# Kernel optimization log

Hardware: AMD Instinct MI355X
Metric: run time of the kernel (lower is better)

Reference implementation:

```python
import jax, jax.numpy as jnp
import numpy as np

B, D, H, E = 1024, 64, 128, 8192


def setup_inputs() -> dict:
    key = jax.random.key(0)
    ks = jax.random.split(key, 10)
    def w(k, shape, fan_in):
        return jax.random.normal(k, shape, jnp.float32) / np.float32(np.sqrt(fan_in))
    return {
        "mu": jax.random.normal(ks[0], (B, D), jnp.float32),
        "current_edge_index": jax.random.randint(ks[1], (2, E), 0, B),
        "W1": w(ks[2], (D, H), D),   "b1": jnp.zeros((H,), jnp.float32),
        "W2": w(ks[3], (H, H), H),   "b2": jnp.zeros((H,), jnp.float32),
        "Ws1": w(ks[4], (2 * H, H), 2 * H), "bs1": jnp.zeros((H,), jnp.float32),
        "Ws2": w(ks[5], (H, 1), H),  "bs2": jnp.zeros((1,), jnp.float32),
        "Wg1": w(ks[6], (2 * H, H), 2 * H), "bg1": jnp.zeros((H,), jnp.float32),
        "Wg2": w(ks[7], (H, D), H), "bg2": jnp.zeros((D,), jnp.float32),
    }


def _gcn(x, W, b, src, dst, n):
    loop = jnp.arange(n)
    s = jnp.concatenate([src, loop])
    d = jnp.concatenate([dst, loop])
    deg = jax.ops.segment_sum(jnp.ones_like(s, x.dtype), d, num_segments=n)
    dinv = jax.lax.rsqrt(jnp.maximum(deg, 1e-12))
    norm = dinv[s] * dinv[d]                      # [E+n]
    xw = x @ W                                    # [n,H]
    out = jax.ops.segment_sum(xw[s] * norm[:, None], d, num_segments=n)
    return out + b


def _pairwise_scores(h, Ws1, bs1, Ws2, bs2):
    # score_mlp([h_i || h_j]) for all pairs, vectorized: split first-layer weight
    A = h @ Ws1[:H]                               # [B,H] contribution of h_i
    C = h @ Ws1[H:]                               # [B,H] contribution of h_j
    pre = jax.nn.relu(A[:, None, :] + C[None, :, :] + bs1)   # [B,B,H]
    s = (pre @ Ws2)[..., 0] + bs2[0]              # [B,B]
    up = jnp.triu(s, 1)                           # only i<j computed in original
    return up + up.T                              # symmetric, zero diagonal


def _kruskal(scores_np, n):
    iu, ju = np.triu_indices(n, 1)
    w = scores_np[iu, ju]
    order = np.argsort(-w, kind="stable")         # descending, stable like list.sort
    parent = list(range(n))
    rank = [0] * n
    def find(u):
        while parent[u] != u:
            parent[u] = parent[parent[u]]
            u = parent[u]
        return u
    edges = []
    for k in order:
        i, j = int(iu[k]), int(ju[k])
        ri, rj = find(i), find(j)
        if ri == rj:
            continue
        if rank[ri] < rank[rj]:
            parent[ri] = rj
        elif rank[ri] > rank[rj]:
            parent[rj] = ri
        else:
            parent[rj] = ri
            rank[ri] += 1
        edges.append((i, j))
        if len(edges) == n - 1:
            break
    return np.asarray(edges, dtype=np.int64)      # [n-1, 2]


def reference(mu, current_edge_index, W1, b1, W2, b2, Ws1, bs1, Ws2, bs2, Wg1, bg1, Wg2, bg2):
    src, dst = current_edge_index[0], current_edge_index[1]
    h = jax.nn.relu(_gcn(mu, W1, b1, src, dst, B))
    h = jax.nn.relu(_gcn(h, W2, b2, src, dst, B))
    scores = _pairwise_scores(h, Ws1, bs1, Ws2, bs2)          # [B,B]
    mst = _kruskal(np.asarray(scores), B)                     # [B-1,2], i<j
    ei = jnp.asarray(mst[:, 0])
    ej = jnp.asarray(mst[:, 1])
    # bidirectional edge index: src=[i,j,...], dst=[j,i,...]
    new_edge_index = jnp.stack([
        jnp.stack([ei, ej], axis=1).reshape(-1),
        jnp.stack([ej, ei], axis=1).reshape(-1),
    ], axis=0)                                                # [2, 2*(B-1)]
    hp = jnp.concatenate([h[ei], h[ej]], axis=1)              # [B-1, 2H]
    gamma = jnp.tanh(jax.nn.relu(hp @ Wg1 + bg1) @ Wg2 + bg2) # [B-1, D]
    return (new_edge_index, gamma)
```

## Files before the change

### kernel.cpp

```cpp
#include <hip/hip_runtime.h>
#include <hip/hip_bf16.h>
#include <math.h>

#define BN 1024
#define DIN 64
#define HD 128
#define EN 8192
#define SLOTS_STRIDE 64
#define MMR 8
#define NC 128

typedef unsigned long long u64;

__global__ void k_init(int* cnt, int* comp, u64* best, int* mstcnt) {
    int i = blockIdx.x * blockDim.x + threadIdx.x;
    if (i < BN) { cnt[i] = 0; comp[i] = i; best[i] = 0ull; }
    if (i == 0) *mstcnt = 0;
}

__global__ void k_fill(const int* dst, int* cnt, int* slots) {
    int e = blockIdx.x * blockDim.x + threadIdx.x;
    if (e < EN) {
        int d = dst[e];
        int p = atomicAdd(&cnt[d], 1);
        if (p < SLOTS_STRIDE) slots[d * SLOTS_STRIDE + p] = e;
    }
}

__global__ __launch_bounds__(128) void k_finish(int* slots, const int* cnt, float* dinv) {
    __shared__ int buf[128][65];
    int tid = threadIdx.x;
    int t = blockIdx.x * 128 + tid;
    int n = cnt[t];
    if (n > SLOTS_STRIDE) n = SLOTS_STRIDE;
    for (int k = 0; k < n; k++) buf[tid][k] = slots[t * SLOTS_STRIDE + k];
    for (int k = 1; k < n; k++) {
        int v = buf[tid][k];
        int q = k - 1;
        while (q >= 0 && buf[tid][q] > v) { buf[tid][q + 1] = buf[tid][q]; q--; }
        buf[tid][q + 1] = v;
    }
    for (int k = 0; k < n; k++) slots[t * SLOTS_STRIDE + k] = buf[tid][k];
    dinv[t] = 1.0f / sqrtf(fmaxf((float)(n + 1), 1e-12f));
}

__global__ __launch_bounds__(128) void k_mm8(const float* x, const float* W, const float* bias,
                                             float* out, int K) {
    __shared__ float xr[MMR][HD];
    int col = threadIdx.x;
    int r0 = blockIdx.x * MMR;
#pragma unroll
    for (int r = 0; r < MMR; r++)
        if (col < K) xr[r][col] = x[(r0 + r) * K + col];
    __syncthreads();
    float b = bias ? bias[col] : 0.0f;
    float acc[MMR];
#pragma unroll
    for (int r = 0; r < MMR; r++) acc[r] = b;
#pragma unroll 4
    for (int k = 0; k < K; k++) {
        float w = W[k * HD + col];
#pragma unroll
        for (int r = 0; r < MMR; r++) acc[r] = fmaf(xr[r][k], w, acc[r]);
    }
#pragma unroll
    for (int r = 0; r < MMR; r++) out[(r0 + r) * HD + col] = acc[r];
}

__global__ __launch_bounds__(128) void k_mmAC(const float* h, const float* Ws1, const float* bs1,
                                              float* Aa, float* Cc) {
    __shared__ float xr[MMR][HD];
    int col = threadIdx.x;
    int r0 = blockIdx.x * MMR;
#pragma unroll
    for (int r = 0; r < MMR; r++) xr[r][col] = h[(r0 + r) * HD + col];
    __syncthreads();
    float accA[MMR], accC[MMR];
    float bc = bs1[col];
#pragma unroll
    for (int r = 0; r < MMR; r++) { accA[r] = 0.0f; accC[r] = bc; }
#pragma unroll 2
    for (int k = 0; k < HD; k++) {
        float wa = Ws1[k * HD + col];
        float wc = Ws1[(HD + k) * HD + col];
#pragma unroll
        for (int r = 0; r < MMR; r++) {
            accA[r] = fmaf(xr[r][k], wa, accA[r]);
            accC[r] = fmaf(xr[r][k], wc, accC[r]);
        }
    }
#pragma unroll
    for (int r = 0; r < MMR; r++) {
        Aa[(r0 + r) * HD + col] = accA[r];
        Cc[(r0 + r) * HD + col] = accC[r];
    }
}

__global__ __launch_bounds__(128) void k_gather(const float* xw, const float* bvec, const int* src,
                                                const int* slots, const int* cnt,
                                                const float* dinv, float* hout) {
    int d = blockIdx.x, t = threadIdx.x;
    float dd = dinv[d];
    float acc = 0.0f;
    int base = d * SLOTS_STRIDE, n = cnt[d];
    if (n > SLOTS_STRIDE) n = SLOTS_STRIDE;
    for (int s = 0; s < n; s++) {
        int e = slots[base + s];
        int sn = src[e];
        acc = fmaf(xw[sn * HD + t], dinv[sn] * dd, acc);
    }
    acc = fmaf(xw[d * HD + t], dd * dd, acc);
    acc += bvec[t];
    hout[d * HD + t] = fmaxf(acc, 0.0f);
}

__global__ __launch_bounds__(256) void k_scores(const float* Aa, const float* Cc,
                                                const float* Ws2, const float* bs2v, float* S) {
    int bi = blockIdx.y, bj = blockIdx.x;
    if (bi > bj) return;
    __shared__ float As[64][68];
    __shared__ float Cs[64][68];
    __shared__ float w2[HD];
    int tid = threadIdx.x;
    int R = bi * 64, Cb = bj * 64;
    if (tid < HD) w2[tid] = Ws2[tid];
    int tx = tid & 15, ty = tid >> 4;
    float acc[4][4] = {};
    for (int half = 0; half < 2; half++) {
        int k0 = half * 64;
        __syncthreads();
        for (int idx = tid; idx < 64 * 64; idx += 256) {
            int row = idx >> 6;
            int kk = idx & 63;
            As[kk][row] = Aa[(R + row) * HD + k0 + kk];
            Cs[kk][row] = Cc[(Cb + row) * HD + k0 + kk];
        }
        __syncthreads();
        for (int kk = 0; kk < 64; kk++) {
            float4 av = *(const float4*)&As[kk][ty * 4];
            float4 cv = *(const float4*)&Cs[kk][tx * 4];
            float wk = w2[k0 + kk];
            float ar[4] = {av.x, av.y, av.z, av.w};
            float cr[4] = {cv.x, cv.y, cv.z, cv.w};
#pragma unroll
            for (int r = 0; r < 4; r++)
#pragma unroll
                for (int q = 0; q < 4; q++) {
                    float tv = fmaxf(ar[r] + cr[q], 0.0f);
                    acc[r][q] = fmaf(tv, wk, acc[r][q]);
                }
        }
    }
    float b2 = bs2v[0];
#pragma unroll
    for (int r = 0; r < 4; r++)
#pragma unroll
        for (int q = 0; q < 4; q++) {
            int gr = R + ty * 4 + r, gc = Cb + tx * 4 + q;
            float v = acc[r][q] + b2;
            if (gr < gc) { S[gr * BN + gc] = v; S[gc * BN + gr] = v; }
            else if (gr == gc) S[gr * BN + gc] = 0.0f;
        }
}

__device__ __forceinline__ u64 edge_key(float w, int i, int j) {
    unsigned u = __float_as_uint(w);
    u = (u & 0x80000000u) ? ~u : (u | 0x80000000u);
    int a = i < j ? i : j, b = i < j ? j : i;
    unsigned packed = (unsigned)(a * BN + b);
    return ((u64)u << 20) | (u64)(0xFFFFFu - packed);
}

__global__ __launch_bounds__(256) void k_best(const float* S, const int* comp,
                                              u64* best, const int* mstcnt) {
    if (*mstcnt >= BN - 1) return;
    int lane = threadIdx.x & 63;
    int i = blockIdx.x * 4 + (threadIdx.x >> 6);
    int ci = comp[i];
    const float* Srow = S + (size_t)i * BN;
    u64 loc = 0ull;
    for (int j = lane; j < BN; j += 64)
        if (comp[j] != ci) {
            u64 key = edge_key(Srow[j], i, j);
            if (key > loc) loc = key;
        }
#pragma unroll
    for (int off = 32; off > 0; off >>= 1) {
        u64 o = __shfl_xor(loc, off);
        if (o > loc) loc = o;
    }
    if (lane == 0 && loc) atomicMax(&best[ci], loc);
}

__global__ __launch_bounds__(1024) void k_merge(int* comp, u64* best, u64* mst, int* mstcnt,
                                                int* compD, int* ncompG, int emitDense) {
    __shared__ int pa[BN], pb[BN];
    int c = threadIdx.x;
    if (*mstcnt >= BN - 1) return;
    int myComp = comp[c];
    bool root = (myComp == c);
    u64 e = best[c];
    int t = c;
    if (root && e) {
        unsigned packed = 0xFFFFFu - (unsigned)(e & 0xFFFFFu);
        int a = packed >> 10, b = packed & 1023;
        int ca = comp[a], cb = comp[b];
        t = (ca == c) ? cb : ca;
    }
    pa[c] = (root && e) ? t : c;
    __syncthreads();
    bool mutual = root && e && (pa[t] == c);
    int p0 = pa[c];
    if (mutual && c < t) p0 = c;
    __syncthreads();
    pa[c] = p0;
    __syncthreads();
    if (root && e && !(mutual && c > t)) {
        int idx = atomicAdd(mstcnt, 1);
        mst[idx] = e;
    }
    for (int it = 0; it < 10; it++) {
        pb[c] = pa[pa[c]];
        __syncthreads();
        pa[c] = pb[c];
        __syncthreads();
    }
    comp[c] = pa[myComp];
    best[c] = 0ull;
    if (!emitDense) return;
    __syncthreads();
    int isR = (comp[c] == c) ? 1 : 0;
    pa[c] = isR;
    __syncthreads();
    for (int d = 1; d < BN; d <<= 1) {
        int v = (c >= d) ? pa[c - d] : 0;
        __syncthreads();
        pa[c] += v;
        __syncthreads();
    }
    if (isR) pb[c] = pa[c] - 1;
    __syncthreads();
    compD[c] = pb[comp[c]];
    if (c == BN - 1) *ncompG = pa[BN - 1];
}

__global__ __launch_bounds__(256) void k_G(const float* S, const int* compD,
                                           const int* mstcnt, u64* G) {
    if (*mstcnt >= BN - 1) return;
    __shared__ u64 t[NC];
    int tid = threadIdx.x;
    int i = blockIdx.x;
    int ci = compD[i];
    if (tid < NC) t[tid] = 0ull;
    __syncthreads();
    const float* Srow = S + (size_t)i * BN;
    for (int j = tid; j < BN; j += 256) {
        int cj = compD[j];
        if (j != i && cj != ci) atomicMax(&t[cj], edge_key(Srow[j], i, j));
    }
    __syncthreads();
    if (tid < NC) G[(size_t)i * NC + tid] = t[tid];
}

__global__ __launch_bounds__(256) void k_Sp(const u64* G, const int* compD,
                                            const int* mstcnt, const int* ncompG, u64* spG) {
    if (*mstcnt >= BN - 1) return;
    int c2 = blockIdx.x;
    int nc = *ncompG;
    if (c2 >= nc) return;
    __shared__ u64 t[NC];
    int tid = threadIdx.x;
    if (tid < NC) t[tid] = 0ull;
    __syncthreads();
    for (int i = tid; i < BN; i += 256) {
        u64 v = G[(size_t)i * NC + c2];
        if (v) atomicMax(&t[compD[i]], v);
    }
    __syncthreads();
    if (tid < NC) spG[(size_t)tid * NC + c2] = t[tid];
}

struct FinSm {
    union {
        u64 sp[NC][NC];
        u64 sk[BN];
    } u;
    int cnd[BN];
    int ccomp[NC], cpa[NC], cpb[NC];
    u64 cbest[NC];
    int lcnt;
};

__global__ __launch_bounds__(1024) void k_mstfin(const u64* spG, const int* compD,
                                                 const int* ncompG, const int* mstcntG,
                                                 u64* mstG, float* out, int* pairs) {
    __shared__ FinSm sm;
    int c = threadIdx.x;
    int total = *mstcntG;
    if (total < BN - 1) {
        int nc = *ncompG;
        for (int idx = c; idx < NC * NC; idx += 1024) ((u64*)sm.u.sp)[idx] = spG[idx];
        sm.cnd[c] = compD[c];
        if (c < NC) { sm.ccomp[c] = c; sm.cbest[c] = 0ull; }
        if (c == 0) sm.lcnt = 0;
        __syncthreads();
        for (int rr = 0; rr < 8 && total < BN - 1; rr++) {
            if (c < nc) {
                int g = sm.ccomp[c];
                u64 m = 0ull;
                for (int c2 = 0; c2 < nc; c2++)
                    if (sm.ccomp[c2] != g) {
                        u64 v = sm.u.sp[c][c2];
                        if (v > m) m = v;
                    }
                if (m) atomicMax(&sm.cbest[g], m);
            }
            __syncthreads();
            if (c < nc) {
                bool root = (sm.ccomp[c] == c);
                u64 e = sm.cbest[c];
                int t2 = c;
                if (root && e) {
                    unsigned packed = 0xFFFFFu - (unsigned)(e & 0xFFFFFu);
                    int a = packed >> 10, b = packed & 1023;
                    int ga = sm.ccomp[sm.cnd[a]], gb = sm.ccomp[sm.cnd[b]];
                    t2 = (ga == c) ? gb : ga;
                }
                sm.cpa[c] = (root && e) ? t2 : c;
            }
            __syncthreads();
            if (c < nc) {
                bool root = (sm.ccomp[c] == c);
                u64 e = sm.cbest[c];
                int t2 = sm.cpa[c];
                bool mutual = root && e && (sm.cpa[t2] == c);
                int p0 = sm.cpa[c];
                if (mutual && c < t2) p0 = c;
                sm.cpb[c] = p0;
                if (root && e && !(mutual && c > t2)) {
                    int idx = total + atomicAdd(&sm.lcnt, 1);
                    mstG[idx] = e;
                }
            }
            __syncthreads();
            if (c < nc) sm.cpa[c] = sm.cpb[c];
            __syncthreads();
            for (int it = 0; it < 7; it++) {
                if (c < nc) sm.cpb[c] = sm.cpa[sm.cpa[c]];
                __syncthreads();
                if (c < nc) sm.cpa[c] = sm.cpb[c];
                __syncthreads();
            }
            if (c < nc) {
                sm.ccomp[c] = sm.cpa[sm.ccomp[c]];
                sm.cbest[c] = 0ull;
            }
            __syncthreads();
            int added = sm.lcnt;
            __syncthreads();
            total += added;
            if (c == 0) sm.lcnt = 0;
            __syncthreads();
        }
    }
    __syncthreads();
    sm.u.sk[c] = (c < BN - 1) ? mstG[c] : 0ull;
    __syncthreads();
    if (c < BN - 1) {
        u64 mykey = sm.u.sk[c];
        int rk = 0;
        for (int f = 0; f < BN - 1; f++) rk += (sm.u.sk[f] > mykey) ? 1 : 0;
        unsigned packed = 0xFFFFFu - (unsigned)(mykey & 0xFFFFFu);
        int i = packed >> 10, j2 = packed & 1023;
        out[2 * rk] = (float)i;
        out[2 * rk + 1] = (float)j2;
        out[2046 + 2 * rk] = (float)j2;
        out[2046 + 2 * rk + 1] = (float)i;
        pairs[2 * rk] = i;
        pairs[2 * rk + 1] = j2;
    }
}

__global__ __launch_bounds__(128) void k_gamma(const float* h, const int* pairs,
                                               const float* Wg1, const float* bg1,
                                               const float* Wg2, const float* bg2, float* out) {
    int eidx = blockIdx.x;
    __shared__ float hp[2 * HD];
    __shared__ float z1[HD];
    int t = threadIdx.x;
    int i = pairs[2 * eidx], j = pairs[2 * eidx + 1];
    hp[t] = h[i * HD + t];
    hp[HD + t] = h[j * HD + t];
    __syncthreads();
    float acc = bg1[t];
    for (int k = 0; k < 2 * HD; k++) acc = fmaf(hp[k], Wg1[k * HD + t], acc);
    z1[t] = fmaxf(acc, 0.0f);
    __syncthreads();
    if (t < DIN) {
        float g = bg2[t];
        for (int k = 0; k < HD; k++) g = fmaf(z1[k], Wg2[k * DIN + t], g);
        out[4092 + eidx * DIN + t] = tanhf(g);
    }
}

extern "C" void kernel_launch(void* const* d_in, const int* in_sizes, int n_in,
                              void* d_out, int out_size, void* d_ws, size_t ws_size,
                              hipStream_t stream) {
    const float* mu  = (const float*)d_in[0];
    const int*   ei  = (const int*)d_in[1];
    const float* W1  = (const float*)d_in[2];
    const float* b1  = (const float*)d_in[3];
    const float* W2  = (const float*)d_in[4];
    const float* b2  = (const float*)d_in[5];
    const float* Ws1 = (const float*)d_in[6];
    const float* bs1 = (const float*)d_in[7];
    const float* Ws2 = (const float*)d_in[8];
    const float* bs2 = (const float*)d_in[9];
    const float* Wg1 = (const float*)d_in[10];
    const float* bg1 = (const float*)d_in[11];
    const float* Wg2 = (const float*)d_in[12];
    const float* bg2 = (const float*)d_in[13];
    float* out = (float*)d_out;

    const int* src = ei;
    const int* dst = ei + EN;

    char* ws = (char*)d_ws;
    int*   slots = (int*)(ws);
    int*   cnt   = (int*)(ws + 262144);
    float* dinv  = (float*)(ws + 266240);
    float* S     = (float*)(ws);
    float* xw    = (float*)(ws + 4194304);
    float* h1    = (float*)(ws + 4718592);
    float* h2    = (float*)(ws + 5242880);
    float* Aa    = (float*)(ws + 5767168);
    float* Cc    = (float*)(ws + 6291456);
    int*   comp  = (int*)(ws + 6815744);
    u64*   best  = (u64*)(ws + 6819840);
    u64*   mstG  = (u64*)(ws + 6828032);
    int*   mstcnt = (int*)(ws + 6836224);
    int*   pairs = (int*)(ws + 6840320);
    int*   compD = (int*)(ws + 6848512);
    int*   ncomp = (int*)(ws + 6852608);
    u64*   G     = (u64*)(ws + 6856704);
    u64*   spG   = (u64*)(ws + 7905280);

    k_init<<<4, 256, 0, stream>>>(cnt, comp, best, mstcnt);
    k_fill<<<EN / 256, 256, 0, stream>>>(dst, cnt, slots);
    k_finish<<<BN / 128, 128, 0, stream>>>(slots, cnt, dinv);

    k_mm8<<<BN / MMR, HD, 0, stream>>>(mu, W1, nullptr, xw, DIN);
    k_gather<<<BN, HD, 0, stream>>>(xw, b1, src, slots, cnt, dinv, h1);
    k_mm8<<<BN / MMR, HD, 0, stream>>>(h1, W2, nullptr, xw, HD);
    k_gather<<<BN, HD, 0, stream>>>(xw, b2, src, slots, cnt, dinv, h2);

    k_mmAC<<<BN / MMR, HD, 0, stream>>>(h2, Ws1, bs1, Aa, Cc);

    k_scores<<<dim3(16, 16), 256, 0, stream>>>(Aa, Cc, Ws2, bs2, S);

    for (int r = 0; r < 3; r++) {
        k_best<<<BN / 4, 256, 0, stream>>>(S, comp, best, mstcnt);
        k_merge<<<1, 1024, 0, stream>>>(comp, best, mstG, mstcnt, compD, ncomp, (r == 2) ? 1 : 0);
    }
    k_G<<<BN, 256, 0, stream>>>(S, compD, mstcnt, G);
    k_Sp<<<NC, 256, 0, stream>>>(G, compD, mstcnt, ncomp, spG);
    k_mstfin<<<1, 1024, 0, stream>>>(spG, compD, ncomp, mstcnt, mstG, out, pairs);

    k_gamma<<<BN - 1, HD, 0, stream>>>(h2, pairs, Wg1, bg1, Wg2, bg2, out);
}
```

Measured before the change: 173.7 us.

## Fuse first Boruvka round into score kernel and merge G/Sp reduction

The score kernel now also computes each node's best edge key through shared-memory row and column atomics followed by global atomicMax. This lets a specialized first merge kernel (every node is its own component) run without a separate k_best pass. The two-stage G then Sp super-graph reduction is folded into one kernel that atomically maxes straight into spG. The init kernel becomes a single memset over a reorganised workspace. Together these remove one full S scan, the G buffer round-trip and a launch, at the cost of extra atomics in the scores epilogue and a fixed 10-iteration pointer jump in merge1.

Result: faster. 162.9 us (-6.2%).

```diff
diff --git a/kernel.cpp b/kernel.cpp
--- a/kernel.cpp
+++ b/kernel.cpp
@@ -11,12 +11,6 @@
 #define NC 128
 
 typedef unsigned long long u64;
-
-__global__ void k_init(int* cnt, int* comp, u64* best, int* mstcnt) {
-    int i = blockIdx.x * blockDim.x + threadIdx.x;
-    if (i < BN) { cnt[i] = 0; comp[i] = i; best[i] = 0ull; }
-    if (i == 0) *mstcnt = 0;
-}
 
 __global__ void k_fill(const int* dst, int* cnt, int* slots) {
     int e = blockIdx.x * blockDim.x + threadIdx.x;
@@ -114,16 +108,27 @@
     hout[d * HD + t] = fmaxf(acc, 0.0f);
 }
 
+__device__ __forceinline__ u64 edge_key(float w, int i, int j) {
+    unsigned u = __float_as_uint(w);
+    u = (u & 0x80000000u) ? ~u : (u | 0x80000000u);
+    int a = i < j ? i : j, b = i < j ? j : i;
+    unsigned packed = (unsigned)(a * BN + b);
+    return ((u64)u << 20) | (u64)(0xFFFFFu - packed);
+}
+
 __global__ __launch_bounds__(256) void k_scores(const float* Aa, const float* Cc,
-                                                const float* Ws2, const float* bs2v, float* S) {
+                                                const float* Ws2, const float* bs2v,
+                                                float* S, u64* best) {
     int bi = blockIdx.y, bj = blockIdx.x;
     if (bi > bj) return;
     __shared__ float As[64][68];
     __shared__ float Cs[64][68];
     __shared__ float w2[HD];
+    __shared__ u64 rmax[64], cmax[64];
     int tid = threadIdx.x;
     int R = bi * 64, Cb = bj * 64;
     if (tid < HD) w2[tid] = Ws2[tid];
+    if (tid < 64) { rmax[tid] = 0ull; cmax[tid] = 0ull; }
     int tx = tid & 15, ty = tid >> 4;
     float acc[4][4] = {};
     for (int half = 0; half < 2; half++) {
@@ -152,23 +157,33 @@
         }
     }
     float b2 = bs2v[0];
+    u64 rloc[4] = {0ull, 0ull, 0ull, 0ull};
+    u64 cloc[4] = {0ull, 0ull, 0ull, 0ull};
 #pragma unroll
     for (int r = 0; r < 4; r++)
 #pragma unroll
         for (int q = 0; q < 4; q++) {
             int gr = R + ty * 4 + r, gc = Cb + tx * 4 + q;
             float v = acc[r][q] + b2;
-            if (gr < gc) { S[gr * BN + gc] = v; S[gc * BN + gr] = v; }
-            else if (gr == gc) S[gr * BN + gc] = 0.0f;
-        }
-}
-
-__device__ __forceinline__ u64 edge_key(float w, int i, int j) {
-    unsigned u = __float_as_uint(w);
-    u = (u & 0x80000000u) ? ~u : (u | 0x80000000u);
-    int a = i < j ? i : j, b = i < j ? j : i;
-    unsigned packed = (unsigned)(a * BN + b);
-    return ((u64)u << 20) | (u64)(0xFFFFFu - packed);
+            if (gr < gc) {
+                S[gr * BN + gc] = v;
+                S[gc * BN + gr] = v;
+                u64 key = edge_key(v, gr, gc);
+                if (key > rloc[r]) rloc[r] = key;
+                if (key > cloc[q]) cloc[q] = key;
+            } else if (gr == gc) S[gr * BN + gc] = 0.0f;
+        }
+#pragma unroll
+    for (int r = 0; r < 4; r++) {
+        if (rloc[r]) atomicMax(&rmax[ty * 4 + r], rloc[r]);
+        if (cloc[r]) atomicMax(&cmax[tx * 4 + r], cloc[r]);
+    }
+    __syncthreads();
+    if (tid < 64) {
+        if (rmax[tid]) atomicMax(&best[R + tid], rmax[tid]);
+    } else if (tid < 128) {
+        if (cmax[tid - 64]) atomicMax(&best[Cb + tid - 64], cmax[tid - 64]);
+    }
 }
 
 __global__ __launch_bounds__(256) void k_best(const float* S, const int* comp,
@@ -190,6 +205,35 @@
         if (o > loc) loc = o;
     }
     if (lane == 0 && loc) atomicMax(&best[ci], loc);
+}
+
+__global__ __launch_bounds__(1024) void k_merge1(u64* best, int* comp, u64* mst, int* mstcnt) {
+    __shared__ int pa[BN], pb[BN];
+    int c = threadIdx.x;
+    u64 e = best[c];
+    unsigned packed = 0xFFFFFu - (unsigned)(e & 0xFFFFFu);
+    int a = packed >> 10, b = packed & 1023;
+    int t = (a == c) ? b : a;
+    pa[c] = t;
+    __syncthreads();
+    bool mutual = (pa[t] == c);
+    int p0 = pa[c];
+    if (mutual && c < t) p0 = c;
+    __syncthreads();
+    pa[c] = p0;
+    __syncthreads();
+    if (!(mutual && c > t)) {
+        int idx = atomicAdd(mstcnt, 1);
+        mst[idx] = e;
+    }
+    for (int it = 0; it < 10; it++) {
+        pb[c] = pa[pa[c]];
+        __syncthreads();
+        pa[c] = pb[c];
+        __syncthreads();
+    }
+    comp[c] = pa[c];
+    best[c] = 0ull;
 }
 
 __global__ __launch_bounds__(1024) void k_merge(int* comp, u64* best, u64* mst, int* mstcnt,
@@ -244,8 +288,8 @@
     if (c == BN - 1) *ncompG = pa[BN - 1];
 }
 
-__global__ __launch_bounds__(256) void k_G(const float* S, const int* compD,
-                                           const int* mstcnt, u64* G) {
+__global__ __launch_bounds__(256) void k_Gsp(const float* S, const int* compD,
+                                             const int* mstcnt, u64* spG) {
     if (*mstcnt >= BN - 1) return;
     __shared__ u64 t[NC];
     int tid = threadIdx.x;
@@ -259,25 +303,7 @@
         if (j != i && cj != ci) atomicMax(&t[cj], edge_key(Srow[j], i, j));
     }
     __syncthreads();
-    if (tid < NC) G[(size_t)i * NC + tid] = t[tid];
-}
-
-__global__ __launch_bounds__(256) void k_Sp(const u64* G, const int* compD,
-                                            const int* mstcnt, const int* ncompG, u64* spG) {
-    if (*mstcnt >= BN - 1) return;
-    int c2 = blockIdx.x;
-    int nc = *ncompG;
-    if (c2 >= nc) return;
-    __shared__ u64 t[NC];
-    int tid = threadIdx.x;
-    if (tid < NC) t[tid] = 0ull;
-    __syncthreads();
-    for (int i = tid; i < BN; i += 256) {
-        u64 v = G[(size_t)i * NC + c2];
-        if (v) atomicMax(&t[compD[i]], v);
-    }
-    __syncthreads();
-    if (tid < NC) spG[(size_t)tid * NC + c2] = t[tid];
+    if (tid < NC && t[tid]) atomicMax(&spG[(size_t)ci * NC + tid], t[tid]);
 }
 
 struct FinSm {
@@ -427,25 +453,25 @@
 
     char* ws = (char*)d_ws;
     int*   slots = (int*)(ws);
-    int*   cnt   = (int*)(ws + 262144);
-    float* dinv  = (float*)(ws + 266240);
     float* S     = (float*)(ws);
     float* xw    = (float*)(ws + 4194304);
     float* h1    = (float*)(ws + 4718592);
     float* h2    = (float*)(ws + 5242880);
     float* Aa    = (float*)(ws + 5767168);
     float* Cc    = (float*)(ws + 6291456);
-    int*   comp  = (int*)(ws + 6815744);
+    int*   cnt   = (int*)(ws + 6815744);
     u64*   best  = (u64*)(ws + 6819840);
-    u64*   mstG  = (u64*)(ws + 6828032);
-    int*   mstcnt = (int*)(ws + 6836224);
-    int*   pairs = (int*)(ws + 6840320);
-    int*   compD = (int*)(ws + 6848512);
-    int*   ncomp = (int*)(ws + 6852608);
-    u64*   G     = (u64*)(ws + 6856704);
-    u64*   spG   = (u64*)(ws + 7905280);
-
-    k_init<<<4, 256, 0, stream>>>(cnt, comp, best, mstcnt);
+    int*   mstcnt = (int*)(ws + 6828032);
+    u64*   spG   = (u64*)(ws + 6832128);
+    int*   comp  = (int*)(ws + 6963200);
+    u64*   mstG  = (u64*)(ws + 6967296);
+    int*   pairs = (int*)(ws + 6975488);
+    int*   compD = (int*)(ws + 6983680);
+    int*   ncomp = (int*)(ws + 6987776);
+    float* dinv  = (float*)(ws + 6991872);
+
+    hipMemsetAsync(ws + 6815744, 0, 147456, stream);
+
     k_fill<<<EN / 256, 256, 0, stream>>>(dst, cnt, slots);
     k_finish<<<BN / 128, 128, 0, stream>>>(slots, cnt, dinv);
 
@@ -456,14 +482,15 @@
 
     k_mmAC<<<BN / MMR, HD, 0, stream>>>(h2, Ws1, bs1, Aa, Cc);
 
-    k_scores<<<dim3(16, 16), 256, 0, stream>>>(Aa, Cc, Ws2, bs2, S);
-
-    for (int r = 0; r < 3; r++) {
-        k_best<<<BN / 4, 256, 0, stream>>>(S, comp, best, mstcnt);
-        k_merge<<<1, 1024, 0, stream>>>(comp, best, mstG, mstcnt, compD, ncomp, (r == 2) ? 1 : 0);
-    }
-    k_G<<<BN, 256, 0, stream>>>(S, compD, mstcnt, G);
-    k_Sp<<<NC, 256, 0, stream>>>(G, compD, mstcnt, ncomp, spG);
+    k_scores<<<dim3(16, 16), 256, 0, stream>>>(Aa, Cc, Ws2, bs2, S, best);
+
+    k_merge1<<<1, 1024, 0, stream>>>(best, comp, mstG, mstcnt);
+    k_best<<<BN / 4, 256, 0, stream>>>(S, comp, best, mstcnt);
+    k_merge<<<1, 1024, 0, stream>>>(comp, best, mstG, mstcnt, compD, ncomp, 0);
+    k_best<<<BN / 4, 256, 0, stream>>>(S, comp, best, mstcnt);
+    k_merge<<<1, 1024, 0, stream>>>(comp, best, mstG, mstcnt, compD, ncomp, 1);
+
+    k_Gsp<<<BN, 256, 0, stream>>>(S, compD, mstcnt, spG);
     k_mstfin<<<1, 1024, 0, stream>>>(spG, compD, ncomp, mstcnt, mstG, out, pairs);
 
     k_gamma<<<BN - 1, HD, 0, stream>>>(h2, pairs, Wg1, bg1, Wg2, bg2, out);
```
